# Kernel tuning notes

Measured on AMD Instinct MI355X. Metric: run time of the kernel, lower is better.

Reference implementation:

```python
import jax, jax.numpy as jnp
import numpy as np

BLOCK = 128
NUM_LEVELS = 16  # 2**num_bits, num_bits=4
FIXED_T = 100.0
EPS = 1e-6


def _blockify(w, B):
    R, C = w.shape
    # [R, C] -> [nb, B, B] with nb = (R//B)*(C//B), row-major block order
    return w.reshape(R // B, B, C // B, B).transpose(0, 2, 1, 3).reshape(-1, B, B)


def _unblockify(blocks, R, C, B):
    return blocks.reshape(R // B, C // B, B, B).transpose(0, 2, 1, 3).reshape(R, C)


def setup_inputs() -> dict:
    key = jax.random.key(0)
    R, C = 4096, 4096
    weight = jax.random.normal(key, (R, C), dtype=jnp.float32)
    blocks = _blockify(weight, BLOCK)
    w_min = blocks.min(axis=(1, 2))  # [nb]
    w_max = blocks.max(axis=(1, 2))  # [nb]
    return {"weight": weight, "w_min": w_min, "w_max": w_max}


def reference(weight, w_min, w_max):
    R, C = weight.shape
    blocks = _blockify(weight, BLOCK)  # [nb, B, B]

    # clamp semantics of the torch code: w_min clamped against detached original
    # w_max; w_max clamped against detached *clamped* w_min (via .item()).
    wmin = jnp.minimum(w_min, jax.lax.stop_gradient(w_max) - EPS)
    wmax = jnp.maximum(w_max, jax.lax.stop_gradient(wmin) + EPS)
    wmin = wmin[:, None, None]
    wmax = wmax[:, None, None]

    scale = wmax - wmin + EPS
    w_norm = (blocks - wmin) / scale                      # [nb, B, B]
    levels = jnp.linspace(0.0, 1.0, NUM_LEVELS, dtype=weight.dtype)  # [L]
    dists = -jnp.abs(w_norm[..., None] - levels)           # [nb, B, B, L]
    soft_probs = jax.nn.softmax(dists * FIXED_T, axis=-1)  # [nb, B, B, L]
    w_q = jnp.sum(soft_probs * levels, axis=-1)            # [nb, B, B]
    w_deq = w_q * (wmax - wmin) + wmin

    # Faithful to torch: sum over dim 0 of each block (its rows) -> [nb, B, L]
    bin_mass = soft_probs.sum(axis=1)
    bin_probs = bin_mass / (bin_mass.sum(axis=(1, 2), keepdims=True) + EPS)
    total_entropy = -jnp.sum(bin_probs * jnp.log(bin_probs + EPS))

    out = _unblockify(w_deq, R, C, BLOCK)
    return out, total_entropy
```

## Files before the change

### kernel.cpp

```cpp
#include <hip/hip_runtime.h>

#define EPS 1e-6f

static constexpr float C2  = 9.617966939259756f;
static constexpr float GC  = 1.2742546176474651e-3f;
static constexpr float C3  = 0.9987273661986602f;
static constexpr float D1  = 511.0f * C3;

typedef float floatx4 __attribute__((ext_vector_type(4)));

#if __has_builtin(__builtin_amdgcn_exp2f)
__device__ __forceinline__ float fast_exp2(float x) { return __builtin_amdgcn_exp2f(x); }
#else
__device__ __forceinline__ float fast_exp2(float x) { return exp2f(x); }
#endif

#if __has_builtin(__builtin_amdgcn_rcpf)
__device__ __forceinline__ float fast_rcp(float x) { return __builtin_amdgcn_rcpf(x); }
#else
__device__ __forceinline__ float fast_rcp(float x) { return 1.0f / x; }
#endif

__device__ __forceinline__ float block_sum_512(float v, float* red, int slot) {
    #pragma unroll
    for (int o = 32; o > 0; o >>= 1) v += __shfl_xor(v, o, 64);
    const int t = threadIdx.x;
    __syncthreads();
    if ((t & 63) == 0) red[slot * 8 + (t >> 6)] = v;
    __syncthreads();
    float s = 0.0f;
    #pragma unroll
    for (int wv = 0; wv < 8; ++wv) s += red[slot * 8 + wv];
    return s;
}

__global__ __launch_bounds__(512, 8) void bq_main_kernel(
    const float* __restrict__ weight,
    const float* __restrict__ w_min,
    const float* __restrict__ w_max,
    float* __restrict__ out,
    float* __restrict__ ent_partial)
{
    __shared__ unsigned int bins[16 * 128];
    __shared__ float red[16];

    const int bid = blockIdx.x;
    const int br = bid >> 5;
    const int bc = bid & 31;
    const int t = threadIdx.x;
    const int cq = t & 31;
    const int rg = t >> 5;
    const int kx = rg & 1;

    #pragma unroll
    for (int i = 0; i < 4; ++i) bins[t + i * 512] = 0u;

    const float wmn = w_min[bid];
    const float wmx = w_max[bid];
    const float lo = fminf(wmn, wmx - EPS);
    const float hi = fmaxf(wmx, lo + EPS);
    const float scale = hi - lo + EPS;
    const float s15 = 15.0f / scale;
    const float dmm15 = (hi - lo) * (1.0f / 15.0f);
    const float tb0 = -lo * s15;
    const float A1 = dmm15;
    const float A2 = dmm15 * (1.0f + 2.0f * GC);
    const float A3 = lo - GC * dmm15;

    __syncthreads();

    const size_t base = (size_t)(br * 128 + rg * 8) * 4096 + (size_t)(bc * 128 + cq * 4);
    const floatx4* __restrict__ wp = (const floatx4*)(weight + base);
    floatx4* __restrict__ op = (floatx4*)(out + base);

    floatx4 w[8];
    #pragma unroll
    for (int i = 0; i < 8; ++i) w[i] = wp[(size_t)i * 1024];

    #define PROC(I, K) do {                                                     \
        const float th = fmaf(w[I][K], s15, tb0);                               \
        const float nf = fminf(fmaxf(floorf(th), 0.0f), 15.0f);                 \
        const int   n  = (int)nf;                                               \
        const float f  = th - nf;                                               \
        const float z  = fast_exp2(fmaf(-2.0f * C2, f, C2));      \
        const float phi = fast_rcp(1.0f + z);                   \
        o4[K] = fmaf(nf, A1, fmaf(phi, A2, A3));                                \
        const unsigned int ui = (unsigned int)fmaf(-phi, D1, D1 + 0.5f);        \
        const unsigned int vi = (unsigned int)fmaf(phi, D1, 0.5f);              \
        atomicAdd(&bins[n * 128 + (K << 5) + cq], ui | (vi << 16));             \
    } while (0)

    #pragma unroll
    for (int i = 0; i < 8; ++i) {
        floatx4 o4;
        if (kx == 0) { PROC(i, 0); PROC(i, 1); PROC(i, 2); PROC(i, 3); }
        else         { PROC(i, 2); PROC(i, 3); PROC(i, 0); PROC(i, 1); }
        __builtin_nontemporal_store(o4, &op[(size_t)i * 1024]);
    }
    #undef PROC

    __syncthreads();

    float s_local = 0.0f, ent = 0.0f;
    float bin[16];
    if (t < 128) {
        unsigned int prev = 0u;
        #pragma unroll
        for (int j = 0; j < 16; ++j) {
            const unsigned int cur = bins[j * 128 + t];
            bin[j] = (float)((cur & 0xFFFFu) + (prev >> 16));
            prev = cur;
            s_local += bin[j];
        }
    }

    const float B = block_sum_512(s_local, red, 0);
    const float invB = fast_rcp(B + EPS);

    if (t < 128) {
        #pragma unroll
        for (int j = 0; j < 16; ++j) {
            const float p = bin[j] * invB;
            ent = fmaf(p, __logf(p + EPS), ent);
        }
    }
    const float entB = block_sum_512(ent, red, 1);
    if (t == 0) ent_partial[bid] = -entB;
}

__global__ __launch_bounds__(64) void bq_ent_reduce(
    const float* __restrict__ part, float* __restrict__ out_ent)
{
    const int t = threadIdx.x;
    float v = 0.0f;
    #pragma unroll
    for (int i = 0; i < 16; ++i) v += part[t + i * 64];
    #pragma unroll
    for (int o = 32; o > 0; o >>= 1) v += __shfl_xor(v, o, 64);
    if (t == 0) out_ent[0] = v;
}

extern "C" void kernel_launch(void* const* d_in, const int* in_sizes, int n_in,
                              void* d_out, int out_size, void* d_ws, size_t ws_size,
                              hipStream_t stream) {
    const float* weight = (const float*)d_in[0];
    const float* wmin = (const float*)d_in[1];
    const float* wmax = (const float*)d_in[2];
    float* out = (float*)d_out;
    float* part = (float*)d_ws;

    bq_main_kernel<<<1024, 512, 0, stream>>>(weight, wmin, wmax, out, part);
    bq_ent_reduce<<<1, 64, 0, stream>>>(part, out + (out_size - 1));
}
```

Baseline: 31.16 us.

## Fuse entropy reduction into main kernel via last-block counter and simplify bin packing

Removes the separate entropy-reduction kernel: each block writes its partial, increments a global counter, and the last block sums all partials. A memset resets the counter each launch. The packed two-halves histogram increment is computed with a single multiply-add, the per-wave atomic reordering is dropped, and an empty asm pins the loads before compute. The constant in the packing changes the low-half encoding and risks a change in the entropy value; the extra memset adds its own launch.

Measured after the change: 69.96 us. 125% more time.

```diff
diff --git a/kernel.cpp b/kernel.cpp
--- a/kernel.cpp
+++ b/kernel.cpp
@@ -39,10 +39,13 @@
     const float* __restrict__ w_min,
     const float* __restrict__ w_max,
     float* __restrict__ out,
-    float* __restrict__ ent_partial)
+    float* __restrict__ ent_partial,
+    unsigned int* __restrict__ done_cnt,
+    float* __restrict__ out_ent)
 {
     __shared__ unsigned int bins[16 * 128];
     __shared__ float red[16];
+    __shared__ unsigned int is_last;
 
     const int bid = blockIdx.x;
     const int br = bid >> 5;
@@ -50,7 +53,6 @@
     const int t = threadIdx.x;
     const int cq = t & 31;
     const int rg = t >> 5;
-    const int kx = rg & 1;
 
     #pragma unroll
     for (int i = 0; i < 4; ++i) bins[t + i * 512] = 0u;
@@ -76,6 +78,8 @@
     floatx4 w[8];
     #pragma unroll
     for (int i = 0; i < 8; ++i) w[i] = wp[(size_t)i * 1024];
+    asm volatile("" : "+v"(w[0]), "+v"(w[1]), "+v"(w[2]), "+v"(w[3]),
+                      "+v"(w[4]), "+v"(w[5]), "+v"(w[6]), "+v"(w[7]));
 
     #define PROC(I, K) do {                                                     \
         const float th = fmaf(w[I][K], s15, tb0);                               \
@@ -85,16 +89,14 @@
         const float z  = fast_exp2(fmaf(-2.0f * C2, f, C2));      \
         const float phi = fast_rcp(1.0f + z);                   \
         o4[K] = fmaf(nf, A1, fmaf(phi, A2, A3));                                \
-        const unsigned int ui = (unsigned int)fmaf(-phi, D1, D1 + 0.5f);        \
         const unsigned int vi = (unsigned int)fmaf(phi, D1, 0.5f);              \
-        atomicAdd(&bins[n * 128 + (K << 5) + cq], ui | (vi << 16));             \
+        atomicAdd(&bins[n * 128 + (K << 5) + cq], vi * 65535u + 510u);          \
     } while (0)
 
     #pragma unroll
     for (int i = 0; i < 8; ++i) {
         floatx4 o4;
-        if (kx == 0) { PROC(i, 0); PROC(i, 1); PROC(i, 2); PROC(i, 3); }
-        else         { PROC(i, 2); PROC(i, 3); PROC(i, 0); PROC(i, 1); }
+        PROC(i, 0); PROC(i, 1); PROC(i, 2); PROC(i, 3);
         __builtin_nontemporal_store(o4, &op[(size_t)i * 1024]);
     }
     #undef PROC
@@ -125,19 +127,25 @@
         }
     }
     const float entB = block_sum_512(ent, red, 1);
-    if (t == 0) ent_partial[bid] = -entB;
-}
 
-__global__ __launch_bounds__(64) void bq_ent_reduce(
-    const float* __restrict__ part, float* __restrict__ out_ent)
-{
-    const int t = threadIdx.x;
-    float v = 0.0f;
-    #pragma unroll
-    for (int i = 0; i < 16; ++i) v += part[t + i * 64];
-    #pragma unroll
-    for (int o = 32; o > 0; o >>= 1) v += __shfl_xor(v, o, 64);
-    if (t == 0) out_ent[0] = v;
+    if (t == 0) {
+        ent_partial[bid] = -entB;
+        __threadfence();
+        const unsigned int prev = atomicAdd(done_cnt, 1u);
+        is_last = (prev == 1023u) ? 1u : 0u;
+    }
+    __syncthreads();
+    if (is_last) {
+        __threadfence();
+        if (t < 64) {
+            float v = 0.0f;
+            #pragma unroll
+            for (int i2 = 0; i2 < 16; ++i2) v += ent_partial[t + i2 * 64];
+            #pragma unroll
+            for (int o = 32; o > 0; o >>= 1) v += __shfl_xor(v, o, 64);
+            if (t == 0) out_ent[0] = v;
+        }
+    }
 }
 
 extern "C" void kernel_launch(void* const* d_in, const int* in_sizes, int n_in,
@@ -148,7 +156,9 @@
     const float* wmax = (const float*)d_in[2];
     float* out = (float*)d_out;
     float* part = (float*)d_ws;
+    unsigned int* cnt = (unsigned int*)((char*)d_ws + 4096);
 
-    bq_main_kernel<<<1024, 512, 0, stream>>>(weight, wmin, wmax, out, part);
-    bq_ent_reduce<<<1, 64, 0, stream>>>(part, out + (out_size - 1));
+    hipMemsetAsync(cnt, 0, sizeof(unsigned int), stream);
+    bq_main_kernel<<<1024, 512, 0, stream>>>(weight, wmin, wmax, out, part,
+                                             cnt, out + (out_size - 1));
 }
```
